# Performance work log

Hardware: AMD Instinct MI355X
Metric: run time of the kernel (lower is better)

The kernel has to match this reference:

```python
import jax, jax.numpy as jnp
import numpy as np

BETA = 0.5
IGNORE_INDEX = -100
TEMPERATURE = 1.0

N, H, V = 2048, 4096, 32000


def setup_inputs() -> dict:
    key = jax.random.key(0)
    k1, k2, k3, k4, k5 = jax.random.split(key, 5)
    scale_s = 1.0 / np.sqrt(H // 2)
    scale_t = 1.0 / np.sqrt(H)
    return {
        "student": jax.random.normal(k1, (N, H // 2), dtype=jnp.float32),
        "W_s": jax.random.normal(k2, (V, H // 2), dtype=jnp.float32) * scale_s,
        "teacher": jax.random.normal(k3, (N, H), dtype=jnp.float32),
        "W_t": jax.random.normal(k4, (V, H), dtype=jnp.float32) * scale_t,
        "target": jax.random.randint(k5, (N,), 0, V, dtype=jnp.int64),
    }


def reference(student, W_s, teacher, W_t, target):
    # Fused linear + JSD: logits are [N, V] (the huge intermediates Liger avoids
    # materializing by chunking over N).
    s_logits = (student @ W_s.T) / TEMPERATURE          # [N, V]  student -> Q
    t_logits = (teacher @ W_t.T) / TEMPERATURE          # [N, V]  teacher -> P
    log_q = jax.nn.log_softmax(s_logits, axis=-1)
    log_p = jax.nn.log_softmax(t_logits, axis=-1)
    p = jnp.exp(log_p)
    q = jnp.exp(log_q)
    # Generalized JSD(beta): beta*KL(P||M) + (1-beta)*KL(Q||M), M = beta*P + (1-beta)*Q
    m = BETA * p + (1.0 - BETA) * q
    log_m = jnp.log(m)
    per_tok = (BETA * jnp.sum(p * (log_p - log_m), axis=-1)
               + (1.0 - BETA) * jnp.sum(q * (log_q - log_m), axis=-1))  # [N]
    mask = target != IGNORE_INDEX
    n_non_ignore = jnp.maximum(jnp.sum(mask), 1)
    loss = jnp.sum(jnp.where(mask, per_tok, 0.0)) / n_non_ignore.astype(per_tok.dtype)
    return loss
```

## Files before the change

### kernel.cpp

```cpp
#include <hip/hip_runtime.h>
#include <hip/hip_bf16.h>
#include <hip/hip_fp8.h>
#include <stdint.h>

#define BETA 0.5f
#define IGNORE_INDEX (-100)
#define WSCALE 64.0f
#define SCALE_ONE  0x7F7F7F7Fu
#define SCALE_D64  0x79797979u

typedef float f32x4 __attribute__((ext_vector_type(4)));
typedef int   i32x4 __attribute__((ext_vector_type(4)));
typedef int   i32x8 __attribute__((ext_vector_type(8)));

__global__ __launch_bounds__(256) void fused_cvt_kernel(
    const float* __restrict__ s0, uint8_t* __restrict__ d0, int e0,
    const float* __restrict__ s1, uint8_t* __restrict__ d1, int e1,
    const float* __restrict__ s2, uint8_t* __restrict__ d2, int e2,
    const float* __restrict__ s3, uint8_t* __restrict__ d3, int eT) {
  for (int c = blockIdx.x; c < eT; c += gridDim.x) {
    const float* src;
    uint8_t* dst;
    float scale;
    int cb = c;
    if (c < e0)      { src = s0; dst = d0; scale = 1.0f;   }
    else if (c < e1) { src = s1; dst = d1; scale = WSCALE; cb -= e0; }
    else if (c < e2) { src = s2; dst = d2; scale = 1.0f;   cb -= e1; }
    else             { src = s3; dst = d3; scale = WSCALE; cb -= e2; }

    const size_t base = (size_t)cb * 8192 + threadIdx.x * 4;
    f32x4 v[8];
#pragma unroll
    for (int k = 0; k < 8; ++k)
      v[k] = __builtin_nontemporal_load(
          reinterpret_cast<const f32x4*>(src + base + k * 1024));
#pragma unroll
    for (int k = 0; k < 8; ++k) {
      int r = 0;
      r = __builtin_amdgcn_cvt_pk_fp8_f32(v[k][0] * scale, v[k][1] * scale, r, false);
      r = __builtin_amdgcn_cvt_pk_fp8_f32(v[k][2] * scale, v[k][3] * scale, r, true);
      *reinterpret_cast<uint32_t*>(dst + base + k * 1024) = (uint32_t)r;
    }
  }
}


__global__ __launch_bounds__(512, 2) void gemm_mx4_kernel(
    const uint8_t* __restrict__ At, const uint8_t* __restrict__ Bt,
    uint16_t* __restrict__ Ct, int Kt,
    const uint8_t* __restrict__ As_, const uint8_t* __restrict__ Bs_,
    uint16_t* __restrict__ Cs, int Ks,
    int V, int RT, int CT) {
  __shared__ __align__(16) uint8_t lds[131072];

  const int half = RT * CT;
  const uint8_t *A, *B;
  uint16_t* C;
  int K, bidx = blockIdx.x;
  if (bidx < half) { A = At; B = Bt; C = Ct; K = Kt; }
  else             { A = As_; B = Bs_; C = Cs; K = Ks; bidx -= half; }

  int L = ((half & 7) == 0) ? ((bidx & 7) * (half >> 3) + (bidx >> 3)) : bidx;
  const int rt = L % RT;
  const int ct = L / RT;
  const int row0 = rt * 256;
  const int col0 = ct * 256;

  const int i  = threadIdx.x;
  const int w  = i >> 6;
  const int l  = i & 63;
  const int wl = l & 15;
  const int kg = l >> 4;
  const int wr = w >> 2;
  const int wc = w & 3;

  const int nJ = K >> 7;

  const int rg = i >> 2;
  const int pq = i & 3;
  const int qlog = pq ^ ((rg >> 1) & 3);
  const uint8_t* aSrc = A + (size_t)(row0 + rg) * K + qlog * 16;
  const uint8_t* bSrc = B + (size_t)(col0 + rg) * K + qlog * 16;
  uint8_t* ldsu = lds;

#define GL(srcp, dstp)                                                     \
  __builtin_amdgcn_global_load_lds(                                        \
      (const __attribute__((address_space(1))) void*)(srcp),               \
      (__attribute__((address_space(3))) void*)(dstp), 16, 0, 0)

#define STAGE_PAIR(P)                                                      \
  do {                                                                     \
    const size_t _kE = (size_t)(2 * (P)) * 64;                             \
    const size_t _kO = (size_t)(2 * (P) + 1) * 64;                         \
    uint8_t* _sb = ldsu + (((P) & 1) * 65536);                             \
    GL(aSrc + _kE, _sb + i * 16);                                          \
    GL(aSrc + _kE + (size_t)128 * K, _sb + i * 16 + 8192);                 \
    GL(aSrc + _kO, _sb + 16384 + i * 16);                                  \
    GL(aSrc + _kO + (size_t)128 * K, _sb + 16384 + i * 16 + 8192);         \
    GL(bSrc + _kE, _sb + 32768 + i * 16);                                  \
    GL(bSrc + _kE + (size_t)128 * K, _sb + 32768 + i * 16 + 8192);         \
    GL(bSrc + _kO, _sb + 49152 + i * 16);                                  \
    GL(bSrc + _kO + (size_t)128 * K, _sb + 49152 + i * 16 + 8192);         \
  } while (0)

  int offA[8], offB[4];
  const int qsw = (kg ^ ((wl >> 1) & 3)) * 16;
#pragma unroll
  for (int m = 0; m < 8; ++m) {
    const int r = wr * 128 + m * 16 + wl;
    offA[m] = r * 64 + qsw;
  }
#pragma unroll
  for (int n = 0; n < 4; ++n) {
    const int r = wc * 64 + n * 16 + wl;
    offB[n] = 32768 + r * 64 + qsw;
  }

  f32x4 acc[8][4] = {};
  i32x8 bF[4];

#define LOADA(dst, mm)                                                     \
  do {                                                                     \
    i32x4 _e = *reinterpret_cast<const i32x4*>(sb + offA[mm]);             \
    i32x4 _o = *reinterpret_cast<const i32x4*>(sb + offA[mm] + 16384);     \
    dst[0] = _e[0]; dst[1] = _e[1]; dst[2] = _e[2]; dst[3] = _e[3];        \
    dst[4] = _o[0]; dst[5] = _o[1]; dst[6] = _o[2]; dst[7] = _o[3];        \
  } while (0)

  STAGE_PAIR(0);
  asm volatile("s_waitcnt vmcnt(0)" ::: "memory");
  __builtin_amdgcn_s_barrier();
  __builtin_amdgcn_sched_barrier(0);

  for (int j = 0; j < nJ; ++j) {
    const uint8_t* sb = lds + (j & 1) * 65536;

#pragma unroll
    for (int n = 0; n < 4; ++n) {
      i32x4 be = *reinterpret_cast<const i32x4*>(sb + offB[n]);
      i32x4 bo = *reinterpret_cast<const i32x4*>(sb + offB[n] + 16384);
      bF[n][0] = be[0]; bF[n][1] = be[1]; bF[n][2] = be[2]; bF[n][3] = be[3];
      bF[n][4] = bo[0]; bF[n][5] = bo[1]; bF[n][6] = bo[2]; bF[n][7] = bo[3];
    }

    if (j + 1 < nJ) STAGE_PAIR(j + 1);

    __builtin_amdgcn_s_setprio(1);
    {
      i32x8 aCur, aNxt;
      LOADA(aCur, 0);
#pragma unroll
      for (int m = 0; m < 8; ++m) {
        if (m + 1 < 8) LOADA(aNxt, m + 1);
#pragma unroll
        for (int n = 0; n < 4; ++n)
          acc[m][n] = __builtin_amdgcn_mfma_scale_f32_16x16x128_f8f6f4(
              aCur, bF[n], acc[m][n], 0, 0, 0, SCALE_ONE, 0, SCALE_D64);
        aCur = aNxt;
      }
    }
    __builtin_amdgcn_s_setprio(0);

    asm volatile("s_waitcnt vmcnt(0)" ::: "memory");
    __builtin_amdgcn_s_barrier();
    __builtin_amdgcn_sched_barrier(0);
  }

#pragma unroll
  for (int mg = 0; mg < 8; ++mg)
#pragma unroll
    for (int ng = 0; ng < 4; ++ng)
#pragma unroll
      for (int r = 0; r < 4; ++r) {
        const int row = row0 + wr * 128 + mg * 16 + kg * 4 + r;
        const int col = col0 + wc * 64 + ng * 16 + wl;
        __hip_bfloat16 bv = __float2bfloat16(acc[mg][ng][r]);
        C[(size_t)row * V + col] = *reinterpret_cast<const uint16_t*>(&bv);
      }
#undef LOADA
#undef STAGE_PAIR
#undef GL
}

__device__ __forceinline__ void unpack8(uint4 v, float* f) {
  uint32_t w[4] = {v.x, v.y, v.z, v.w};
#pragma unroll
  for (int j = 0; j < 4; ++j) {
    union { uint32_t u; float x; } lo, hi;
    lo.u = (w[j] & 0xffffu) << 16;
    hi.u = w[j] & 0xffff0000u;
    f[2 * j] = lo.x;
    f[2 * j + 1] = hi.x;
  }
}

__device__ __forceinline__ float blockReduce(float v, float* sh) {
#pragma unroll
  for (int o = 32; o >= 1; o >>= 1) v += __shfl_xor(v, o, 64);
  const int w = threadIdx.x >> 6;
  __syncthreads();
  if ((threadIdx.x & 63) == 0) sh[w] = v;
  __syncthreads();
  float r = sh[0];
#pragma unroll
  for (int i = 1; i < 4; ++i) r += sh[i];
  return r;
}

__global__ __launch_bounds__(256) void jsd_rows_kernel(
    const uint16_t* __restrict__ SL, const uint16_t* __restrict__ TL,
    float* __restrict__ per_tok, int V) {
  __shared__ __align__(16) uint16_t rowS[32000];
  __shared__ __align__(16) uint16_t rowT[32000];
  __shared__ float redM[2][4], redS[2][4], red[4];

  const int t = threadIdx.x;
  const int row = blockIdx.x;
  const uint4* gS = reinterpret_cast<const uint4*>(SL + (size_t)row * V);
  const uint4* gT = reinterpret_cast<const uint4*>(TL + (size_t)row * V);
  uint4* lS = reinterpret_cast<uint4*>(rowS);
  uint4* lT = reinterpret_cast<uint4*>(rowT);
  const int nvec = V >> 3;

  float mS = -3.0e38f, sS = 0.f, mT = -3.0e38f, sT = 0.f;
  for (int i = t; i < nvec; i += 256) {
    uint4 vs = gS[i], vt = gT[i];
    lS[i] = vs; lT[i] = vt;
    float fs[8], ft[8];
    unpack8(vs, fs);
    unpack8(vt, ft);
    float vmS = fs[0], vmT = ft[0];
#pragma unroll
    for (int j = 1; j < 8; ++j) { vmS = fmaxf(vmS, fs[j]); vmT = fmaxf(vmT, ft[j]); }
    if (vmS > mS) { sS *= __expf(mS - vmS); mS = vmS; }
    if (vmT > mT) { sT *= __expf(mT - vmT); mT = vmT; }
#pragma unroll
    for (int j = 0; j < 8; ++j) { sS += __expf(fs[j] - mS); sT += __expf(ft[j] - mT); }
  }

#pragma unroll
  for (int o = 32; o >= 1; o >>= 1) {
    float mo = __shfl_xor(mS, o, 64), so = __shfl_xor(sS, o, 64);
    float mn = fmaxf(mS, mo);
    sS = sS * __expf(mS - mn) + so * __expf(mo - mn); mS = mn;
    mo = __shfl_xor(mT, o, 64); so = __shfl_xor(sT, o, 64);
    mn = fmaxf(mT, mo);
    sT = sT * __expf(mT - mn) + so * __expf(mo - mn); mT = mn;
  }
  const int wv = t >> 6;
  if ((t & 63) == 0) {
    redM[0][wv] = mS; redS[0][wv] = sS;
    redM[1][wv] = mT; redS[1][wv] = sT;
  }
  __syncthreads();
  float M0 = redM[0][0], S0 = redS[0][0];
  float M1 = redM[1][0], S1 = redS[1][0];
#pragma unroll
  for (int k = 1; k < 4; ++k) {
    float m2 = redM[0][k], s2 = redS[0][k];
    float mn = fmaxf(M0, m2);
    S0 = S0 * __expf(M0 - mn) + s2 * __expf(m2 - mn); M0 = mn;
    m2 = redM[1][k]; s2 = redS[1][k];
    mn = fmaxf(M1, m2);
    S1 = S1 * __expf(M1 - mn) + s2 * __expf(m2 - mn); M1 = mn;
  }
  const float lseS = M0 + __logf(S0);
  const float lseT = M1 + __logf(S1);

  float acc = 0.f;
  for (int i = t; i < nvec; i += 256) {
    float fs[8], ft[8];
    unpack8(lS[i], fs);
    unpack8(lT[i], ft);
#pragma unroll
    for (int j = 0; j < 8; ++j) {
      const float lq = fs[j] - lseS;
      const float lp = ft[j] - lseT;
      const float q = __expf(lq);
      const float p = __expf(lp);
      const float m = BETA * p + (1.f - BETA) * q;
      const float lm = __logf(m);
      acc += BETA * p * (lp - lm) + (1.f - BETA) * q * (lq - lm);
    }
  }
  acc = blockReduce(acc, red);
  if (t == 0) per_tok[row] = acc;
}

__global__ __launch_bounds__(256) void finalize_kernel(
    const float* __restrict__ per_tok, const int* __restrict__ tgt,
    float* __restrict__ out, int N) {
  __shared__ float redf[4];
  __shared__ int redi[4];
  float s = 0.f;
  int c = 0;
  for (int i = threadIdx.x; i < N; i += 256) {
    if (tgt[i] != IGNORE_INDEX) { s += per_tok[i]; c += 1; }
  }
#pragma unroll
  for (int o = 32; o >= 1; o >>= 1) {
    s += __shfl_xor(s, o, 64);
    c += __shfl_xor(c, o, 64);
  }
  const int w = threadIdx.x >> 6;
  if ((threadIdx.x & 63) == 0) { redf[w] = s; redi[w] = c; }
  __syncthreads();
  if (threadIdx.x == 0) {
    float st = 0.f;
    int ct = 0;
#pragma unroll
    for (int i = 0; i < 4; ++i) { st += redf[i]; ct += redi[i]; }
    out[0] = st / (float)(ct > 0 ? ct : 1);
  }
}

extern "C" void kernel_launch(void* const* d_in, const int* in_sizes, int n_in,
                              void* d_out, int out_size, void* d_ws, size_t ws_size,
                              hipStream_t stream) {
  const float* student = (const float*)d_in[0];
  const float* W_s     = (const float*)d_in[1];
  const float* teacher = (const float*)d_in[2];
  const float* W_t     = (const float*)d_in[3];
  const int*   target  = (const int*)d_in[4];

  const int N  = in_sizes[4];
  const int Hs = in_sizes[0] / N;
  const int Ht = in_sizes[2] / N;
  const int V  = in_sizes[1] / Hs;

  char* ws = (char*)d_ws;
  size_t off = 0;
  auto alloc = [&](size_t bytes) -> void* {
    void* p = ws + off;
    off += (bytes + 255) & ~(size_t)255;
    return p;
  };
  uint8_t* Sf8  = (uint8_t*)alloc((size_t)N * Hs);
  uint8_t* Wsf8 = (uint8_t*)alloc((size_t)V * Hs);
  uint8_t* Tf8  = (uint8_t*)alloc((size_t)N * Ht);
  uint8_t* Wtf8 = (uint8_t*)alloc((size_t)V * Ht);
  uint16_t* slog = (uint16_t*)alloc((size_t)N * V * 2);
  uint16_t* tlog = (uint16_t*)alloc((size_t)N * V * 2);
  float* per_tok = (float*)alloc((size_t)N * sizeof(float));
  (void)ws_size;

  const int c0 = (N * Hs) / 8192;
  const int c1 = c0 + (V * Hs) / 8192;
  const int c2 = c1 + (N * Ht) / 8192;
  const int cT = c2 + (V * Ht) / 8192;
  fused_cvt_kernel<<<4096, 256, 0, stream>>>(
      student, Sf8, c0, W_s, Wsf8, c1, teacher, Tf8, c2, W_t, Wtf8, cT);

  const int RT = N / 256;
  const int CT = V / 256;
  gemm_mx4_kernel<<<2 * RT * CT, 512, 0, stream>>>(
      Tf8, Wtf8, tlog, Ht, Sf8, Wsf8, slog, Hs, V, RT, CT);

  jsd_rows_kernel<<<N, 256, 0, stream>>>(slog, tlog, per_tok, V);
  finalize_kernel<<<1, 256, 0, stream>>>(per_tok, target, (float*)d_out, N);
}
```

Before: 725.7 us.

## Prefetch next-stage B fragments mid-loop and widen fp8 conversion stores

The GEMM main loop now waits for the next stage's global loads partway through the MFMA sequence (after row group 4). It then reads the next B fragments from LDS into a second register set, so the B LDS reads of the next iteration overlap with the remaining MFMAs instead of sitting at the top of the loop. This adds eight i32x8 registers of pressure at two waves per SIMD and moves a barrier into the middle of the compute. Separately, the fp8 conversion kernel now has each thread handle 16 contiguous floats and write 16-byte stores instead of scattered 4-byte stores.

```diff
diff --git a/kernel.cpp b/kernel.cpp
--- a/kernel.cpp
+++ b/kernel.cpp
@@ -28,24 +28,33 @@
     else if (c < e2) { src = s2; dst = d2; scale = 1.0f;   cb -= e1; }
     else             { src = s3; dst = d3; scale = WSCALE; cb -= e2; }
 
-    const size_t base = (size_t)cb * 8192 + threadIdx.x * 4;
+    const size_t base = (size_t)cb * 8192 + threadIdx.x * 16;
     f32x4 v[8];
 #pragma unroll
-    for (int k = 0; k < 8; ++k)
+    for (int k = 0; k < 4; ++k)
       v[k] = __builtin_nontemporal_load(
-          reinterpret_cast<const f32x4*>(src + base + k * 1024));
-#pragma unroll
-    for (int k = 0; k < 8; ++k) {
+          reinterpret_cast<const f32x4*>(src + base + k * 4));
+#pragma unroll
+    for (int k = 0; k < 4; ++k)
+      v[4 + k] = __builtin_nontemporal_load(
+          reinterpret_cast<const f32x4*>(src + base + 4096 + k * 4));
+
+    auto pack4 = [&scale](const f32x4& x) -> uint32_t {
       int r = 0;
-      r = __builtin_amdgcn_cvt_pk_fp8_f32(v[k][0] * scale, v[k][1] * scale, r, false);
-      r = __builtin_amdgcn_cvt_pk_fp8_f32(v[k][2] * scale, v[k][3] * scale, r, true);
-      *reinterpret_cast<uint32_t*>(dst + base + k * 1024) = (uint32_t)r;
-    }
-  }
-}
-
-
-__global__ __launch_bounds__(512, 2) void gemm_mx4_kernel(
+      r = __builtin_amdgcn_cvt_pk_fp8_f32(x[0] * scale, x[1] * scale, r, false);
+      r = __builtin_amdgcn_cvt_pk_fp8_f32(x[2] * scale, x[3] * scale, r, true);
+      return (uint32_t)r;
+    };
+    uint4 o0, o1;
+    o0.x = pack4(v[0]); o0.y = pack4(v[1]); o0.z = pack4(v[2]); o0.w = pack4(v[3]);
+    o1.x = pack4(v[4]); o1.y = pack4(v[5]); o1.z = pack4(v[6]); o1.w = pack4(v[7]);
+    *reinterpret_cast<uint4*>(dst + base)        = o0;
+    *reinterpret_cast<uint4*>(dst + base + 4096) = o1;
+  }
+}
+
+
+__global__ __launch_bounds__(512, 2) void gemm_mx5_kernel(
     const uint8_t* __restrict__ At, const uint8_t* __restrict__ Bt,
     uint16_t* __restrict__ Ct, int Kt,
     const uint8_t* __restrict__ As_, const uint8_t* __restrict__ Bs_,
@@ -117,53 +126,74 @@
   }
 
   f32x4 acc[8][4] = {};
-  i32x8 bF[4];
-
-#define LOADA(dst, mm)                                                     \
+  i32x8 bF[4], bN[4];
+
+#define LOADA(dst, sp, mm)                                                 \
   do {                                                                     \
-    i32x4 _e = *reinterpret_cast<const i32x4*>(sb + offA[mm]);             \
-    i32x4 _o = *reinterpret_cast<const i32x4*>(sb + offA[mm] + 16384);     \
+    i32x4 _e = *reinterpret_cast<const i32x4*>((sp) + offA[mm]);           \
+    i32x4 _o = *reinterpret_cast<const i32x4*>((sp) + offA[mm] + 16384);   \
     dst[0] = _e[0]; dst[1] = _e[1]; dst[2] = _e[2]; dst[3] = _e[3];        \
     dst[4] = _o[0]; dst[5] = _o[1]; dst[6] = _o[2]; dst[7] = _o[3];        \
+  } while (0)
+
+#define READB(dst, sp)                                                     \
+  do {                                                                     \
+    _Pragma("unroll")                                                      \
+    for (int _n = 0; _n < 4; ++_n) {                                       \
+      i32x4 _be = *reinterpret_cast<const i32x4*>((sp) + offB[_n]);        \
+      i32x4 _bo = *reinterpret_cast<const i32x4*>((sp) + offB[_n] + 16384);\
+      dst[_n][0] = _be[0]; dst[_n][1] = _be[1];                            \
+      dst[_n][2] = _be[2]; dst[_n][3] = _be[3];                            \
+      dst[_n][4] = _bo[0]; dst[_n][5] = _bo[1];                            \
+      dst[_n][6] = _bo[2]; dst[_n][7] = _bo[3];                            \
+    }                                                                      \
   } while (0)
 
   STAGE_PAIR(0);
   asm volatile("s_waitcnt vmcnt(0)" ::: "memory");
   __builtin_amdgcn_s_barrier();
   __builtin_amdgcn_sched_barrier(0);
+  READB(bF, lds);
 
   for (int j = 0; j < nJ; ++j) {
     const uint8_t* sb = lds + (j & 1) * 65536;
-
-#pragma unroll
-    for (int n = 0; n < 4; ++n) {
-      i32x4 be = *reinterpret_cast<const i32x4*>(sb + offB[n]);
-      i32x4 bo = *reinterpret_cast<const i32x4*>(sb + offB[n] + 16384);
-      bF[n][0] = be[0]; bF[n][1] = be[1]; bF[n][2] = be[2]; bF[n][3] = be[3];
-      bF[n][4] = bo[0]; bF[n][5] = bo[1]; bF[n][6] = bo[2]; bF[n][7] = bo[3];
-    }
-
-    if (j + 1 < nJ) STAGE_PAIR(j + 1);
+    const uint8_t* so = lds + ((j + 1) & 1) * 65536;
+    const bool more = (j + 1) < nJ;
+
+    if (more) STAGE_PAIR(j + 1);
 
     __builtin_amdgcn_s_setprio(1);
     {
       i32x8 aCur, aNxt;
-      LOADA(aCur, 0);
+      LOADA(aCur, sb, 0);
 #pragma unroll
       for (int m = 0; m < 8; ++m) {
-        if (m + 1 < 8) LOADA(aNxt, m + 1);
+        if (m + 1 < 8) LOADA(aNxt, sb, m + 1);
 #pragma unroll
         for (int n = 0; n < 4; ++n)
           acc[m][n] = __builtin_amdgcn_mfma_scale_f32_16x16x128_f8f6f4(
               aCur, bF[n], acc[m][n], 0, 0, 0, SCALE_ONE, 0, SCALE_D64);
+        if (m == 4 && more) {
+          __builtin_amdgcn_s_setprio(0);
+          asm volatile("s_waitcnt vmcnt(0)" ::: "memory");
+          __builtin_amdgcn_s_barrier();
+          __builtin_amdgcn_sched_barrier(0);
+          READB(bN, so);
+          __builtin_amdgcn_s_setprio(1);
+        }
         aCur = aNxt;
       }
     }
     __builtin_amdgcn_s_setprio(0);
 
-    asm volatile("s_waitcnt vmcnt(0)" ::: "memory");
+    if (!more) asm volatile("s_waitcnt vmcnt(0)" ::: "memory");
     __builtin_amdgcn_s_barrier();
     __builtin_amdgcn_sched_barrier(0);
+
+    if (more) {
+#pragma unroll
+      for (int n = 0; n < 4; ++n) bF[n] = bN[n];
+    }
   }
 
 #pragma unroll
@@ -177,6 +207,7 @@
         __hip_bfloat16 bv = __float2bfloat16(acc[mg][ng][r]);
         C[(size_t)row * V + col] = *reinterpret_cast<const uint16_t*>(&bv);
       }
+#undef READB
 #undef LOADA
 #undef STAGE_PAIR
 #undef GL
@@ -353,7 +384,7 @@
 
   const int RT = N / 256;
   const int CT = V / 256;
-  gemm_mx4_kernel<<<2 * RT * CT, 512, 0, stream>>>(
+  gemm_mx5_kernel<<<2 * RT * CT, 512, 0, stream>>>(
       Tf8, Wtf8, tlog, Ht, Sf8, Wsf8, slog, Hs, V, RT, CT);
 
   jsd_rows_kernel<<<N, 256, 0, stream>>>(slog, tlog, per_tok, V);
```

Result: slower. 2.030 ms (+179.7%).
